# Kernel optimization log

Measured on AMD Instinct MI355X. Metric: run time of the kernel, lower is better.

## Reference

```python
import jax, jax.numpy as jnp
import numpy as np

K_NEIGHBORS = 8

def _mlp(x, W0, b0, W1, b1, W2, b2, W3, b3):
    # FCBlock(hidden=128, num_hidden_layers=2, in=D+3, out=D, outermost_linear=True, with_ln=False)
    h = jax.nn.relu(x @ W0 + b0)
    h = jax.nn.relu(h @ W1 + b1)
    h = jax.nn.relu(h @ W2 + b2)
    return h @ W3 + b3


def setup_inputs() -> dict:
    key = jax.random.key(0)
    ks = jax.random.split(key, 8)
    N, M, D, H = 6890, 32768, 64, 128  # vertices, query pts, latent dim, hidden
    Din = D + 3
    sc = 0.05
    return {
        "vertex": jax.random.normal(ks[0], (N, 3), jnp.float32),
        "vertex_features": jax.random.normal(ks[1], (N, D), jnp.float32),
        "query_pts": jax.random.normal(ks[2], (M, 3), jnp.float32),
        "W0": jax.random.normal(ks[3], (Din, H), jnp.float32) * sc,
        "b0": jnp.zeros((H,), jnp.float32),
        "W1": jax.random.normal(ks[4], (H, H), jnp.float32) * sc,
        "b1": jnp.zeros((H,), jnp.float32),
        "W2": jax.random.normal(ks[5], (H, H), jnp.float32) * sc,
        "b2": jnp.zeros((H,), jnp.float32),
        "W3": jax.random.normal(ks[6], (H, D), jnp.float32) * sc,
        "b3": jnp.zeros((D,), jnp.float32),
    }


def reference(vertex, vertex_features, query_pts, W0, b0, W1, b1, W2, b2, W3, b3):
    # --- KNN: k smallest euclidean distances from each query to vertices ---
    # squared distance matrix [M, N] via the expanded form (single GEMM)
    d2 = (jnp.sum(query_pts * query_pts, axis=-1, keepdims=True)
          - 2.0 * (query_pts @ vertex.T)
          + jnp.sum(vertex * vertex, axis=-1))
    neg_d2, k_index = jax.lax.top_k(-d2, K_NEIGHBORS)  # ascending distances, [M,K]
    k_dist = jnp.sqrt(jnp.maximum(-neg_d2, 0.0)) + 1e-9
    # F.normalize(1/d, p=1, dim=1): inverse-distance weights, L1-normalized over k
    inv = 1.0 / k_dist
    k_weight = inv / jnp.sum(inv, axis=1, keepdims=True)  # [M,K]
    # --- gather neighbors ---
    k_vertices = vertex[k_index]                 # [M,K,3]
    k_nearest_features = vertex_features[k_index]  # [M,K,D]
    k_nearest_vector = query_pts[:, None, :] - k_vertices  # [M,K,3]
    vector_input = jnp.concatenate([k_nearest_features, k_nearest_vector], axis=-1)  # [M,K,D+3]
    # --- small MLP + distance-weighted reduction over neighbors ---
    features = _mlp(vector_input, W0, b0, W1, b1, W2, b2, W3, b3)  # [M,K,D]
    return jnp.sum(features * k_weight[..., None], axis=1)  # [M,D]
```

## Files before the change

### kernel.cpp

```cpp
#include <hip/hip_runtime.h>
#include <hip/hip_fp16.h>

#define NV    6890
#define NQ    32768
#define DF    64
#define NW    16
#define CHUNK 431
#define SAMP  32
#define CAPQ  20

typedef _Float16 v8h  __attribute__((ext_vector_type(8)));
typedef float    f32x4 __attribute__((ext_vector_type(4)));
typedef unsigned int       u32;
typedef unsigned long long u64;
typedef unsigned short     u16;

static constexpr size_t VTX4_OFF  = 0;
static constexpr size_t KIDX_OFF  = 110592;
static constexpr size_t KW_OFF    = KIDX_OFF + (size_t)NQ * 8 * 4;
static constexpr size_t WFRAG_OFF = KW_OFF + (size_t)NQ * 8 * 4;

__device__ __forceinline__ u32 monof(float s) {
    u32 u = __float_as_uint(s);
    return (u & 0x80000000u) ? ~u : (u | 0x80000000u);
}

#define DINSERT(sv) do {                                               \
    bool c0 = (sv) < dbest[0], c1 = (sv) < dbest[1],                   \
         c2 = (sv) < dbest[2], c3 = (sv) < dbest[3],                   \
         c4 = (sv) < dbest[4], c5 = (sv) < dbest[5],                   \
         c6 = (sv) < dbest[6], c7 = (sv) < dbest[7];                   \
    dbest[7] = c7 ? (c6 ? dbest[6] : (sv)) : dbest[7];                 \
    dbest[6] = c6 ? (c5 ? dbest[5] : (sv)) : dbest[6];                 \
    dbest[5] = c5 ? (c4 ? dbest[4] : (sv)) : dbest[5];                 \
    dbest[4] = c4 ? (c3 ? dbest[3] : (sv)) : dbest[4];                 \
    dbest[3] = c3 ? (c2 ? dbest[2] : (sv)) : dbest[3];                 \
    dbest[2] = c2 ? (c1 ? dbest[1] : (sv)) : dbest[2];                 \
    dbest[1] = c1 ? (c0 ? dbest[0] : (sv)) : dbest[1];                 \
    dbest[0] = c0 ? (sv) : dbest[0];                                   \
} while (0)

#define KINSERT(nk) do {                                  \
    bool c0 = (nk) < key[0], c1 = (nk) < key[1],          \
         c2 = (nk) < key[2], c3 = (nk) < key[3],          \
         c4 = (nk) < key[4], c5 = (nk) < key[5],          \
         c6 = (nk) < key[6], c7 = (nk) < key[7];          \
    key[7] = c7 ? (c6 ? key[6] : (nk)) : key[7];          \
    key[6] = c6 ? (c5 ? key[5] : (nk)) : key[6];          \
    key[5] = c5 ? (c4 ? key[4] : (nk)) : key[5];          \
    key[4] = c4 ? (c3 ? key[3] : (nk)) : key[4];          \
    key[3] = c3 ? (c2 ? key[2] : (nk)) : key[3];          \
    key[2] = c2 ? (c1 ? key[1] : (nk)) : key[2];          \
    key[1] = c1 ? (c0 ? key[0] : (nk)) : key[1];          \
    key[0] = c0 ? (nk) : key[0];                          \
} while (0)

#define TRYQ(sv, jv) do {                                                      \
    if ((sv) <= T) {                                                           \
        if (cnt < CAPQ) { qq[w][l][cnt] = (u16)(jv); ++cnt; }                  \
        else {                                                                 \
            u64 nk = ((u64)monof(sv) << 16) | (u64)(jv);                       \
            if (nk < key[7]) { KINSERT(nk); }                                  \
        }                                                                      \
    }                                                                          \
} while (0)

__global__ void prep_kernel(const float* __restrict__ vtx, float4* __restrict__ vtx4,
                            const float* __restrict__ W0, const float* __restrict__ W1,
                            const float* __restrict__ W2, const float* __restrict__ W3,
                            _Float16* __restrict__ wfrag) {
    int b = blockIdx.x;
    if (b < 27) {
        int i = b * 256 + threadIdx.x;
        if (i < NV) {
            float x = vtx[i * 3 + 0], y = vtx[i * 3 + 1], z = vtx[i * 3 + 2];
            vtx4[i] = make_float4(x, y, z, 0.5f * (x * x + y * y + z * z));
        }
        return;
    }
    int e = (b - 27) * 256 + threadIdx.x;
    const float* W; int base, NCT, C, KD;
    if      (e < 12288) { W = W0; base = 0;     NCT = 8; C = 128; KD = 67;  }
    else if (e < 28672) { W = W1; base = 12288; NCT = 8; C = 128; KD = 128; }
    else if (e < 45056) { W = W2; base = 28672; NCT = 8; C = 128; KD = 128; }
    else                { W = W3; base = 45056; NCT = 4; C = 64;  KD = 128; }
    int le = e - base;
    int t = le >> 9, r = le & 511;
    int lane = r >> 3, j = r & 7;
    int kt = t / NCT, ct = t % NCT;
    int k = kt * 32 + (lane >> 4) * 8 + j;
    int col = ct * 16 + (lane & 15);
    float v = (k < KD) ? W[k * C + col] : 0.0f;
    wfrag[e] = (_Float16)v;
}

__device__ __forceinline__ float vdist(const float4 v, float nqx, float nqy, float nqz) {
    float s = fmaf(nqx, v.x, v.w);
    s = fmaf(nqy, v.y, s);
    return fmaf(nqz, v.z, s);
}

__global__ __launch_bounds__(1024, 8) void knn_kernel(const float4* __restrict__ vtx4,
                                                      const float* __restrict__ qpts,
                                                      int* __restrict__ kidx,
                                                      float* __restrict__ kw) {
    __shared__ u64   kbuf[8][64][9];
    __shared__ u16   qq[NW][64][CAPQ];
    __shared__ float Tbc[64];
    float (*fbuf)[64][9] = (float (*)[64][9])kbuf;

    const int tid = threadIdx.x, w = tid >> 6, l = tid & 63;
    const int m = blockIdx.x * 64 + l;
    const float qx = qpts[m * 3 + 0], qy = qpts[m * 3 + 1], qz = qpts[m * 3 + 2];
    const float nqx = -qx, nqy = -qy, nqz = -qz;

    float dbest[8];
#pragma unroll
    for (int i = 0; i < 8; ++i) dbest[i] = 3.0e38f;
    {
        const int s0 = w * SAMP;
#pragma unroll 4
        for (int j = s0; j < s0 + SAMP; ++j) {
            float s = vdist(vtx4[j], nqx, nqy, nqz);
            DINSERT(s);
        }
    }
#pragma unroll
    for (int i = 0; i < 8; ++i) fbuf[w][l][i] = dbest[i];
    __syncthreads();

#pragma unroll 1
    for (int st = 8; st >= 1; st >>= 1) {
        if (w < st) {
#pragma unroll
            for (int e = 0; e < 8; ++e) {
                float s = fbuf[w + st][l][e];
                if (s < dbest[7]) { DINSERT(s); }
            }
            if (st > 1) {
#pragma unroll
                for (int i = 0; i < 8; ++i) fbuf[w][l][i] = dbest[i];
            }
        }
        __syncthreads();
    }
    if (w == 0) Tbc[l] = dbest[7];
    __syncthreads();
    const float T = Tbc[l];

    u64 key[8];
#pragma unroll
    for (int i = 0; i < 8; ++i) key[i] = ~0ull;
    u32 cnt = 0;
    {
        const int j0 = w * CHUNK;
        const int j1 = (j0 + CHUNK < NV) ? j0 + CHUNK : NV;
        int j = j0;
#pragma unroll 1
        for (; j + 4 <= j1; j += 4) {
            float4 v0 = vtx4[j], v1 = vtx4[j + 1], v2 = vtx4[j + 2], v3 = vtx4[j + 3];
            float s0 = vdist(v0, nqx, nqy, nqz);
            float s1 = vdist(v1, nqx, nqy, nqz);
            float s2 = vdist(v2, nqx, nqy, nqz);
            float s3 = vdist(v3, nqx, nqy, nqz);
            TRYQ(s0, j); TRYQ(s1, j + 1); TRYQ(s2, j + 2); TRYQ(s3, j + 3);
        }
        for (; j < j1; ++j) {
            float s = vdist(vtx4[j], nqx, nqy, nqz);
            TRYQ(s, j);
        }
    }

#pragma unroll 1
    for (int b = 0; b < CAPQ; b += 4) {
        if (!__any(cnt > (u32)b)) break;
        u32 jj[4]; float4 vv[4];
#pragma unroll
        for (int t = 0; t < 4; ++t) {
            u32 qi = ((u32)(b + t) < cnt) ? (u32)qq[w][l][b + t] : 0u;
            jj[t] = qi; vv[t] = vtx4[qi];
        }
#pragma unroll
        for (int t = 0; t < 4; ++t) {
            float s = vdist(vv[t], nqx, nqy, nqz);
            u64 nk = ((u64)monof(s) << 16) | (u64)jj[t];
            nk = ((u32)(b + t) < cnt) ? nk : ~0ull;
            if (nk < key[7]) { KINSERT(nk); }
        }
    }

#pragma unroll 1
    for (int st = 8; st >= 1; st >>= 1) {
        if (w >= st && w < 2 * st) {
#pragma unroll
            for (int i = 0; i < 8; ++i) kbuf[w - st][l][i] = key[i];
        }
        __syncthreads();
        if (w < st) {
#pragma unroll
            for (int e = 0; e < 8; ++e) {
                u64 nk = kbuf[w][l][e];
                if (nk < key[7]) { KINSERT(nk); }
            }
        }
        __syncthreads();
    }

    if (w == 0) {
        float q2 = fmaf(qx, qx, fmaf(qy, qy, qz * qz));
        float inv[8], ssum = 0.0f;
        int idx8[8];
#pragma unroll
        for (int i = 0; i < 8; ++i) {
            u32 us = (u32)(key[i] >> 16);
            u32 uo = (us & 0x80000000u) ? (us & 0x7FFFFFFFu) : ~us;
            float s = __uint_as_float(uo);
            float dd = fmaf(2.0f, s, q2);
            float d = sqrtf(fmaxf(dd, 0.0f)) + 1e-9f;
            inv[i] = 1.0f / d; ssum += inv[i];
            idx8[i] = (int)(key[i] & 0xFFFFull);
        }
        float rs = 1.0f / ssum;
#pragma unroll
        for (int i = 0; i < 8; ++i) {
            kidx[m * 8 + i] = idx8[i];
            kw[m * 8 + i]   = inv[i] * rs;
        }
    }
}

template <int KSTEPS, int NCT, bool RELU>
__device__ __forceinline__ void mlp_layer(_Float16 (*buf)[136],
                                          const _Float16* __restrict__ frag,
                                          const float* __restrict__ bias,
                                          int w, int l) {
    const int cl = l & 15, gl = l >> 4;
    f32x4 acc[2][NCT];
#pragma unroll
    for (int ct = 0; ct < NCT; ++ct) {
        float bv = bias[ct * 16 + cl];
#pragma unroll
        for (int rt = 0; rt < 2; ++rt) acc[rt][ct] = (f32x4){bv, bv, bv, bv};
    }
    const _Float16* fb = frag + (size_t)l * 8;
#pragma unroll 1
    for (int ks = 0; ks < KSTEPS; ++ks) {
        v8h a0 = *(const v8h*)&buf[w * 32 + cl][ks * 32 + gl * 8];
        v8h a1 = *(const v8h*)&buf[w * 32 + 16 + cl][ks * 32 + gl * 8];
#pragma unroll
        for (int ct = 0; ct < NCT; ++ct) {
            v8h bf = *(const v8h*)(fb + (size_t)(ks * NCT + ct) * 512);
            acc[0][ct] = __builtin_amdgcn_mfma_f32_16x16x32_f16(a0, bf, acc[0][ct], 0, 0, 0);
            acc[1][ct] = __builtin_amdgcn_mfma_f32_16x16x32_f16(a1, bf, acc[1][ct], 0, 0, 0);
        }
    }
#pragma unroll
    for (int rt = 0; rt < 2; ++rt)
#pragma unroll
        for (int ct = 0; ct < NCT; ++ct)
#pragma unroll
            for (int j = 0; j < 4; ++j) {
                float v = acc[rt][ct][j];
                if (RELU) v = fmaxf(v, 0.0f);
                buf[w * 32 + rt * 16 + gl * 4 + j][ct * 16 + cl] = (_Float16)v;
            }
}

__global__ __launch_bounds__(256, 3) void mlp_kernel(
    const float* __restrict__ vf, const float4* __restrict__ vtx4,
    const float* __restrict__ qpts,
    const int* __restrict__ kidx, const float* __restrict__ kw,
    const _Float16* __restrict__ wfrag,
    const float* __restrict__ b0, const float* __restrict__ b1,
    const float* __restrict__ b2, const float* __restrict__ b3,
    float* __restrict__ out) {
    __shared__ _Float16 buf[128][136];
    const int tid = threadIdx.x, w = tid >> 6, l = tid & 63;
    {
        int h = l & 1;
        int lrow = w * 32 + (l >> 1);
        int grow = blockIdx.x * 128 + lrow;
        int q = grow >> 3;
        int idx = kidx[grow];
        const float4* src = (const float4*)(vf + (size_t)idx * DF) + h * 8;
#pragma unroll
        for (int t = 0; t < 4; ++t) {
            float4 a = src[2 * t], b = src[2 * t + 1];
            v8h pk = {(_Float16)a.x, (_Float16)a.y, (_Float16)a.z, (_Float16)a.w,
                      (_Float16)b.x, (_Float16)b.y, (_Float16)b.z, (_Float16)b.w};
            *(v8h*)&buf[lrow][h * 32 + t * 8] = pk;
        }
        v8h zz = {0, 0, 0, 0, 0, 0, 0, 0};
        if (h == 0) {
            float4 v = vtx4[idx];
            float qx = qpts[q * 3 + 0], qy = qpts[q * 3 + 1], qz = qpts[q * 3 + 2];
            v8h d = {(_Float16)(qx - v.x), (_Float16)(qy - v.y), (_Float16)(qz - v.z),
                     0, 0, 0, 0, 0};
            *(v8h*)&buf[lrow][64] = d;
            *(v8h*)&buf[lrow][88] = zz;
        } else {
            *(v8h*)&buf[lrow][72] = zz;
            *(v8h*)&buf[lrow][80] = zz;
        }
    }

    mlp_layer<3, 8, true>(buf, wfrag + 0,     b0, w, l);
    mlp_layer<4, 8, true>(buf, wfrag + 12288, b1, w, l);
    mlp_layer<4, 8, true>(buf, wfrag + 28672, b2, w, l);

    {
        const int cl = l & 15, gl = l >> 4;
        f32x4 acc[2][4];
#pragma unroll
        for (int ct = 0; ct < 4; ++ct) {
            float bv = b3[ct * 16 + cl];
#pragma unroll
            for (int rt = 0; rt < 2; ++rt) acc[rt][ct] = (f32x4){bv, bv, bv, bv};
        }
        const _Float16* fb = wfrag + 45056 + (size_t)l * 8;
#pragma unroll 1
        for (int ks = 0; ks < 4; ++ks) {
            v8h a0 = *(const v8h*)&buf[w * 32 + cl][ks * 32 + gl * 8];
            v8h a1 = *(const v8h*)&buf[w * 32 + 16 + cl][ks * 32 + gl * 8];
#pragma unroll
            for (int ct = 0; ct < 4; ++ct) {
                v8h bf = *(const v8h*)(fb + (size_t)(ks * 4 + ct) * 512);
                acc[0][ct] = __builtin_amdgcn_mfma_f32_16x16x32_f16(a0, bf, acc[0][ct], 0, 0, 0);
                acc[1][ct] = __builtin_amdgcn_mfma_f32_16x16x32_f16(a1, bf, acc[1][ct], 0, 0, 0);
            }
        }
        int GRbase = blockIdx.x * 128 + w * 32;
#pragma unroll
        for (int rt = 0; rt < 2; ++rt) {
            int r4 = GRbase + rt * 16 + gl * 4;
            float4 kv = *(const float4*)&kw[r4];
#pragma unroll
            for (int ct = 0; ct < 4; ++ct) {
                float v = acc[rt][ct][0] * kv.x + acc[rt][ct][1] * kv.y +
                          acc[rt][ct][2] * kv.z + acc[rt][ct][3] * kv.w;
                v += __shfl_xor(v, 16);
                if ((gl & 1) == 0) {
                    int q = (GRbase + rt * 16 + ((gl == 2) ? 8 : 0)) >> 3;
                    out[(size_t)q * 64 + ct * 16 + cl] = v;
                }
            }
        }
    }
}

extern "C" void kernel_launch(void* const* d_in, const int* in_sizes, int n_in,
                              void* d_out, int out_size, void* d_ws, size_t ws_size,
                              hipStream_t stream) {
    const float* vtx = (const float*)d_in[0];
    const float* vf  = (const float*)d_in[1];
    const float* qp  = (const float*)d_in[2];
    const float* W0  = (const float*)d_in[3];
    const float* b0  = (const float*)d_in[4];
    const float* W1  = (const float*)d_in[5];
    const float* b1  = (const float*)d_in[6];
    const float* W2  = (const float*)d_in[7];
    const float* b2  = (const float*)d_in[8];
    const float* W3  = (const float*)d_in[9];
    const float* b3  = (const float*)d_in[10];
    float*       out = (float*)d_out;

    char*      ws    = (char*)d_ws;
    float4*    vtx4  = (float4*)(ws + VTX4_OFF);
    int*       kidx  = (int*)(ws + KIDX_OFF);
    float*     kw    = (float*)(ws + KW_OFF);
    _Float16*  wfrag = (_Float16*)(ws + WFRAG_OFF);

    hipLaunchKernelGGL(prep_kernel, dim3(27 + 208), dim3(256), 0, stream,
                       vtx, vtx4, W0, W1, W2, W3, wfrag);
    hipLaunchKernelGGL(knn_kernel, dim3(NQ / 64), dim3(1024), 0, stream, vtx4, qp, kidx, kw);
    hipLaunchKernelGGL(mlp_kernel, dim3(NQ * 8 / 128), dim3(256), 0, stream,
                       vf, vtx4, qp, kidx, kw, wfrag, b0, b1, b2, b3, out);
}
```

Before: 189.1 us.

## Branchless KNN candidate buffering with overflow rescan; move weight prep into KNN launch

```diff
diff --git a/kernel.cpp b/kernel.cpp
--- a/kernel.cpp
+++ b/kernel.cpp
@@ -55,43 +55,18 @@
     key[0] = c0 ? (nk) : key[0];                          \
 } while (0)
 
-#define TRYQ(sv, jv) do {                                                      \
-    if ((sv) <= T) {                                                           \
-        if (cnt < CAPQ) { qq[w][l][cnt] = (u16)(jv); ++cnt; }                  \
-        else {                                                                 \
-            u64 nk = ((u64)monof(sv) << 16) | (u64)(jv);                       \
-            if (nk < key[7]) { KINSERT(nk); }                                  \
-        }                                                                      \
-    }                                                                          \
+#define TRYB(sv, jv) do {                                 \
+    u32 pos = cnt < CAPQ ? cnt : CAPQ;                    \
+    qq[w][l][pos] = (u16)(jv);                            \
+    cnt += ((sv) <= T) ? 1u : 0u;                         \
 } while (0)
 
-__global__ void prep_kernel(const float* __restrict__ vtx, float4* __restrict__ vtx4,
-                            const float* __restrict__ W0, const float* __restrict__ W1,
-                            const float* __restrict__ W2, const float* __restrict__ W3,
-                            _Float16* __restrict__ wfrag) {
-    int b = blockIdx.x;
-    if (b < 27) {
-        int i = b * 256 + threadIdx.x;
-        if (i < NV) {
-            float x = vtx[i * 3 + 0], y = vtx[i * 3 + 1], z = vtx[i * 3 + 2];
-            vtx4[i] = make_float4(x, y, z, 0.5f * (x * x + y * y + z * z));
-        }
-        return;
-    }
-    int e = (b - 27) * 256 + threadIdx.x;
-    const float* W; int base, NCT, C, KD;
-    if      (e < 12288) { W = W0; base = 0;     NCT = 8; C = 128; KD = 67;  }
-    else if (e < 28672) { W = W1; base = 12288; NCT = 8; C = 128; KD = 128; }
-    else if (e < 45056) { W = W2; base = 28672; NCT = 8; C = 128; KD = 128; }
-    else                { W = W3; base = 45056; NCT = 4; C = 64;  KD = 128; }
-    int le = e - base;
-    int t = le >> 9, r = le & 511;
-    int lane = r >> 3, j = r & 7;
-    int kt = t / NCT, ct = t % NCT;
-    int k = kt * 32 + (lane >> 4) * 8 + j;
-    int col = ct * 16 + (lane & 15);
-    float v = (k < KD) ? W[k * C + col] : 0.0f;
-    wfrag[e] = (_Float16)v;
+__global__ void prep_kernel(const float* __restrict__ vtx, float4* __restrict__ vtx4) {
+    int i = blockIdx.x * 256 + threadIdx.x;
+    if (i < NV) {
+        float x = vtx[i * 3 + 0], y = vtx[i * 3 + 1], z = vtx[i * 3 + 2];
+        vtx4[i] = make_float4(x, y, z, 0.5f * (x * x + y * y + z * z));
+    }
 }
 
 __device__ __forceinline__ float vdist(const float4 v, float nqx, float nqy, float nqz) {
@@ -103,9 +78,32 @@
 __global__ __launch_bounds__(1024, 8) void knn_kernel(const float4* __restrict__ vtx4,
                                                       const float* __restrict__ qpts,
                                                       int* __restrict__ kidx,
-                                                      float* __restrict__ kw) {
+                                                      float* __restrict__ kw,
+                                                      const float* __restrict__ W0,
+                                                      const float* __restrict__ W1,
+                                                      const float* __restrict__ W2,
+                                                      const float* __restrict__ W3,
+                                                      _Float16* __restrict__ wfrag) {
+    if (blockIdx.x >= NQ / 64) {
+        int e = (blockIdx.x - NQ / 64) * 1024 + threadIdx.x;
+        const float* W; int base, NCT, C, KD;
+        if      (e < 12288) { W = W0; base = 0;     NCT = 8; C = 128; KD = 67;  }
+        else if (e < 28672) { W = W1; base = 12288; NCT = 8; C = 128; KD = 128; }
+        else if (e < 45056) { W = W2; base = 28672; NCT = 8; C = 128; KD = 128; }
+        else                { W = W3; base = 45056; NCT = 4; C = 64;  KD = 128; }
+        int le = e - base;
+        int t = le >> 9, r = le & 511;
+        int lane = r >> 3, jj = r & 7;
+        int kt = t / NCT, ct = t % NCT;
+        int k = kt * 32 + (lane >> 4) * 8 + jj;
+        int col = ct * 16 + (lane & 15);
+        float v = (k < KD) ? W[k * C + col] : 0.0f;
+        wfrag[e] = (_Float16)v;
+        return;
+    }
+
     __shared__ u64   kbuf[8][64][9];
-    __shared__ u16   qq[NW][64][CAPQ];
+    __shared__ u16   qq[NW][64][CAPQ + 1];
     __shared__ float Tbc[64];
     float (*fbuf)[64][9] = (float (*)[64][9])kbuf;
 
@@ -152,22 +150,43 @@
 #pragma unroll
     for (int i = 0; i < 8; ++i) key[i] = ~0ull;
     u32 cnt = 0;
+    const int j0 = w * CHUNK;
+    const int j1 = (j0 + CHUNK < NV) ? j0 + CHUNK : NV;
     {
-        const int j0 = w * CHUNK;
-        const int j1 = (j0 + CHUNK < NV) ? j0 + CHUNK : NV;
         int j = j0;
 #pragma unroll 1
-        for (; j + 4 <= j1; j += 4) {
-            float4 v0 = vtx4[j], v1 = vtx4[j + 1], v2 = vtx4[j + 2], v3 = vtx4[j + 3];
-            float s0 = vdist(v0, nqx, nqy, nqz);
-            float s1 = vdist(v1, nqx, nqy, nqz);
-            float s2 = vdist(v2, nqx, nqy, nqz);
-            float s3 = vdist(v3, nqx, nqy, nqz);
-            TRYQ(s0, j); TRYQ(s1, j + 1); TRYQ(s2, j + 2); TRYQ(s3, j + 3);
+        for (; j + 8 <= j1; j += 8) {
+            float4 va = vtx4[j + 0], vb = vtx4[j + 1], vc = vtx4[j + 2], vd = vtx4[j + 3];
+            float4 ve = vtx4[j + 4], vf = vtx4[j + 5], vg = vtx4[j + 6], vh = vtx4[j + 7];
+            float s0 = vdist(va, nqx, nqy, nqz);
+            float s1 = vdist(vb, nqx, nqy, nqz);
+            float s2 = vdist(vc, nqx, nqy, nqz);
+            float s3 = vdist(vd, nqx, nqy, nqz);
+            float s4 = vdist(ve, nqx, nqy, nqz);
+            float s5 = vdist(vf, nqx, nqy, nqz);
+            float s6 = vdist(vg, nqx, nqy, nqz);
+            float s7 = vdist(vh, nqx, nqy, nqz);
+            TRYB(s0, j + 0); TRYB(s1, j + 1); TRYB(s2, j + 2); TRYB(s3, j + 3);
+            TRYB(s4, j + 4); TRYB(s5, j + 5); TRYB(s6, j + 6); TRYB(s7, j + 7);
         }
         for (; j < j1; ++j) {
             float s = vdist(vtx4[j], nqx, nqy, nqz);
-            TRYQ(s, j);
+            TRYB(s, j);
+        }
+    }
+
+    if (__any(cnt > CAPQ)) {
+        bool ovf = cnt > CAPQ;
+        if (ovf) cnt = 0;
+#pragma unroll 1
+        for (int j = j0; j < j1; ++j) {
+            if (ovf) {
+                float s = vdist(vtx4[j], nqx, nqy, nqz);
+                if (s <= T) {
+                    u64 nk = ((u64)monof(s) << 16) | (u64)j;
+                    if (nk < key[7]) { KINSERT(nk); }
+                }
+            }
         }
     }
 
@@ -370,9 +389,9 @@
     float*     kw    = (float*)(ws + KW_OFF);
     _Float16*  wfrag = (_Float16*)(ws + WFRAG_OFF);
 
-    hipLaunchKernelGGL(prep_kernel, dim3(27 + 208), dim3(256), 0, stream,
-                       vtx, vtx4, W0, W1, W2, W3, wfrag);
-    hipLaunchKernelGGL(knn_kernel, dim3(NQ / 64), dim3(1024), 0, stream, vtx4, qp, kidx, kw);
+    hipLaunchKernelGGL(prep_kernel, dim3(27), dim3(256), 0, stream, vtx, vtx4);
+    hipLaunchKernelGGL(knn_kernel, dim3(NQ / 64 + 52), dim3(1024), 0, stream,
+                       vtx4, qp, kidx, kw, W0, W1, W2, W3, wfrag);
     hipLaunchKernelGGL(mlp_kernel, dim3(NQ * 8 / 128), dim3(256), 0, stream,
                        vf, vtx4, qp, kidx, kw, wfrag, b0, b1, b2, b3, out);
 }
```

After: 239.6 us. 1.27x slower.
